# Kernel optimization log

Hardware: AMD Instinct MI355X
Metric: run time of the kernel (lower is better)

Reference implementation:

```python
import jax, jax.numpy as jnp
import numpy as np

G, N, D, H = 2, 192, 64, 4
DK = D // H


def setup_inputs() -> dict:
    key = jax.random.key(0)
    ks = jax.random.split(key, 9)
    s = 0.05
    return {
        "adj": jax.random.normal(ks[0], (G, N, N, D), dtype=jnp.float32),
        "Wq": jax.random.normal(ks[1], (D, D), dtype=jnp.float32) * s,
        "bq": jax.random.normal(ks[2], (D,), dtype=jnp.float32) * s,
        "Wk": jax.random.normal(ks[3], (D, D), dtype=jnp.float32) * s,
        "bk": jax.random.normal(ks[4], (D,), dtype=jnp.float32) * s,
        "Wv": jax.random.normal(ks[5], (D, D), dtype=jnp.float32) * s,
        "bv": jax.random.normal(ks[6], (D,), dtype=jnp.float32) * s,
        "Wo": jax.random.normal(ks[7], (D, D), dtype=jnp.float32) * s,
        "bo": jax.random.normal(ks[8], (D,), dtype=jnp.float32) * s,
    }


def _proj_heads(x, W, b):
    # x: (G,N,N,D) -> (G,N,H,N,DK); W stored as (in,out)
    y = jnp.einsum('gnmd,de->gnme', x, W) + b
    g, n, m, _ = y.shape
    return y.reshape(g, n, m, H, DK).transpose(0, 1, 3, 2, 4)


def reference(adj, Wq, bq, Wk, bk, Wv, bv, Wo, bo):
    q = _proj_heads(adj, Wq, bq)  # (G,N,H,N,DK)
    k = _proj_heads(adj, Wk, bk)
    v = _proj_heads(adj, Wv, bv)
    scores = jnp.einsum('gnhtd,gnhsd->gnhts', q, k) / jnp.sqrt(jnp.float32(DK))
    p = jax.nn.softmax(scores, axis=-1)  # (G,N,H,N,N)
    x = jnp.einsum('gnhts,gnhsd->gnhtd', p, v)  # (G,N,H,N,DK)
    x = x.transpose(0, 1, 3, 2, 4).reshape(adj.shape[0], adj.shape[1], -1, H * DK)
    return jnp.einsum('gnmd,de->gnme', x, Wo) + bo
```

## Files before the change

kernel.cpp:

```cpp
#include <hip/hip_runtime.h>


typedef float    f32x4 __attribute__((ext_vector_type(4)));
typedef float    f32x2 __attribute__((ext_vector_type(2)));
typedef _Float16 f16x2 __attribute__((ext_vector_type(2)));
typedef _Float16 f16x4 __attribute__((ext_vector_type(4)));
typedef _Float16 f16x8 __attribute__((ext_vector_type(8)));

__device__ __forceinline__ int xsw64(int r, int c) {
    return (r << 6) + (((c >> 3) ^ (r & 7)) << 3) + (c & 7);
}
__device__ __forceinline__ int vsw192(int r, int c) {
    return r * 192 + ((((c >> 3) ^ (r & 7)) & 31) << 3) + (c & 7);
}

#define QSCALE 0.36067376022224085f

extern "C" __global__ void spa_prep(const float* __restrict__ Wq, const float* __restrict__ bq,
                                    const float* __restrict__ Wk, const float* __restrict__ bk,
                                    const float* __restrict__ Wv, const float* __restrict__ bv,
                                    const float* __restrict__ Wo, const float* __restrict__ bo,
                                    _Float16* __restrict__ WT, float* __restrict__ BS) {
    const int t = blockIdx.x * 256 + threadIdx.x;
    const int m  = t >> 10;
    const int e  = (t >> 4) & 63;
    const int d0 = (t & 15) << 2;
    const float* W[4] = {Wq, Wk, Wv, Wo};
    const float s = (m == 0) ? QSCALE : 1.0f;
    f16x4 h4;
#pragma unroll
    for (int j = 0; j < 4; ++j) h4[j] = (_Float16)(W[m][(d0 + j) * 64 + e] * s);
    *(f16x4*)&WT[(m << 12) + (e << 6) + d0] = h4;
    if (t < 256) {
        const int mm = t >> 6, ee = t & 63;
        const float* B[4] = {bq, bk, bv, bo};
        BS[t] = B[mm][ee] * ((mm == 0) ? QSCALE : 1.0f);
    }
}

extern "C" __global__ void __launch_bounds__(512, 6)
spa_mfma3(const float* __restrict__ adj,
          const _Float16* __restrict__ WTg, const float* __restrict__ BS,
          float* __restrict__ out) {
    extern __shared__ __align__(16) char smem[];
    _Float16* X  = (_Float16*)smem;
    _Float16* VT = (_Float16*)smem + 12288;

    const int tid  = threadIdx.x;
    const int l    = tid & 63;
    const int wv   = tid >> 6;
    const int l15  = l & 15;
    const int g    = l >> 4;
    const int gn   = blockIdx.x >> 1;
    const int half = blockIdx.x & 1;
    const int ttb  = half * 6;

    const float* Xg   = adj + (size_t)gn * (192 * 64);
    float*       outg = out + (size_t)gn * (192 * 64);

    const int h  = wv >> 1;
    const int eh = h << 4;
    const int et = wv & 3;

    const f16x8 wv0 = *(const f16x8*)&WTg[(2 << 12) + (((et << 4) + l15) << 6) + (g << 3)];
    const f16x8 wv1 = *(const f16x8*)&WTg[(2 << 12) + (((et << 4) + l15) << 6) + 32 + (g << 3)];
    const f16x8 wk0 = *(const f16x8*)&WTg[(1 << 12) + ((eh + l15) << 6) + (g << 3)];
    const f16x8 wk1 = *(const f16x8*)&WTg[(1 << 12) + ((eh + l15) << 6) + 32 + (g << 3)];
    const f16x8 wq0 = *(const f16x8*)&WTg[(0 << 12) + ((eh + l15) << 6) + (g << 3)];
    const f16x8 wq1 = *(const f16x8*)&WTg[(0 << 12) + ((eh + l15) << 6) + 32 + (g << 3)];
    const f32x4 bv4 = *(const f32x4*)&BS[128 + (et << 4) + (g << 2)];
    const f32x4 bk4 = *(const f32x4*)&BS[64 + eh + (g << 2)];
    const f32x4 bq4 = *(const f32x4*)&BS[0 + eh + (g << 2)];

    {
        const int d0 = (tid & 7) << 3;
        const int t0 = tid >> 3;
#pragma unroll
        for (int p = 0; p < 3; ++p) {
            int t = t0 + (p << 6);
            const float4* src = (const float4*)&Xg[(t << 6) + d0];
            float4 v0 = src[0], v1 = src[1];
            f16x8 h8;
            h8[0]=(_Float16)v0.x; h8[1]=(_Float16)v0.y; h8[2]=(_Float16)v0.z; h8[3]=(_Float16)v0.w;
            h8[4]=(_Float16)v1.x; h8[5]=(_Float16)v1.y; h8[6]=(_Float16)v1.z; h8[7]=(_Float16)v1.w;
            *(f16x8*)&X[xsw64(t, d0)] = h8;
        }
    }
    __syncthreads();

    const f32x4 z = {0.f, 0.f, 0.f, 0.f};

    {
        const int stb = (wv >> 2) * 6;
        for (int s6 = 0; s6 < 6; ++s6) {
            int st = stb + s6;
            f16x8 x0 = *(const f16x8*)&X[xsw64((st << 4) + l15, g << 3)];
            f16x8 x1 = *(const f16x8*)&X[xsw64((st << 4) + l15, 32 + (g << 3))];
            f32x4 c = __builtin_amdgcn_mfma_f32_16x16x32_f16(wv0, x0, z, 0, 0, 0);
            c = __builtin_amdgcn_mfma_f32_16x16x32_f16(wv1, x1, c, 0, 0, 0);
            int s = (st << 4) + l15;
#pragma unroll
            for (int r = 0; r < 4; ++r)
                VT[vsw192((et << 4) + (g << 2) + r, s)] = (_Float16)(c[r] + bv4[r]);
        }
    }

    f16x4 kf[12];
#pragma unroll
    for (int st = 0; st < 12; ++st) {
        f16x8 x0 = *(const f16x8*)&X[xsw64((st << 4) + l15, g << 3)];
        f16x8 x1 = *(const f16x8*)&X[xsw64((st << 4) + l15, 32 + (g << 3))];
        f32x4 c = __builtin_amdgcn_mfma_f32_16x16x32_f16(wk0, x0, z, 0, 0, 0);
        c = __builtin_amdgcn_mfma_f32_16x16x32_f16(wk1, x1, c, 0, 0, 0);
#pragma unroll
        for (int r = 0; r < 4; ++r) kf[st][r] = (_Float16)(c[r] + bk4[r]);
    }

    f16x4 qf[3];
    const int tloc = (wv & 1) * 3;
#pragma unroll
    for (int j = 0; j < 3; ++j) {
        int tt = ttb + tloc + j;
        f16x8 x0 = *(const f16x8*)&X[xsw64((tt << 4) + l15, g << 3)];
        f16x8 x1 = *(const f16x8*)&X[xsw64((tt << 4) + l15, 32 + (g << 3))];
        f32x4 c = __builtin_amdgcn_mfma_f32_16x16x32_f16(wq0, x0, z, 0, 0, 0);
        c = __builtin_amdgcn_mfma_f32_16x16x32_f16(wq1, x1, c, 0, 0, 0);
#pragma unroll
        for (int r = 0; r < 4; ++r) qf[j][r] = (_Float16)(c[r] + bq4[r]);
    }
    __syncthreads();

    f16x4 vf[12];
#pragma unroll
    for (int st = 0; st < 12; ++st)
        vf[st] = *(const f16x4*)&VT[vsw192(eh + l15, (st << 4) + (g << 2))];

    for (int j = 0; j < 3; ++j) {
        f32x4 accA = z, accB = z;
        f32x2 rs = {0.f, 0.f};
#pragma unroll
        for (int st = 0; st < 12; ++st) {
            f32x4 c = __builtin_amdgcn_mfma_f32_16x16x16f16(kf[st], qf[j], z, 0, 0, 0);
            float p0 = exp2f(c[0]), p1 = exp2f(c[1]);
            float p2 = exp2f(c[2]), p3 = exp2f(c[3]);
            rs += (f32x2){p0, p1} + (f32x2){p2, p3};
            f16x2 lo = __builtin_bit_cast(f16x2, __builtin_amdgcn_cvt_pkrtz(p0, p1));
            f16x2 hi = __builtin_bit_cast(f16x2, __builtin_amdgcn_cvt_pkrtz(p2, p3));
            f16x4 pf = __builtin_shufflevector(lo, hi, 0, 1, 2, 3);
            if (st & 1) accB = __builtin_amdgcn_mfma_f32_16x16x16f16(vf[st], pf, accB, 0, 0, 0);
            else        accA = __builtin_amdgcn_mfma_f32_16x16x16f16(vf[st], pf, accA, 0, 0, 0);
        }
        float rsum = rs[0] + rs[1];
        rsum += __shfl_xor(rsum, 16);
        rsum += __shfl_xor(rsum, 32);
        const float rinv = 1.0f / rsum;
        f16x4 o4;
#pragma unroll
        for (int r = 0; r < 4; ++r) o4[r] = (_Float16)((accA[r] + accB[r]) * rinv);
        *(f16x4*)&X[xsw64(((ttb + tloc + j) << 4) + l15, eh + (g << 2))] = o4;
    }
    __syncthreads();

    {
        const int eo = ((wv & 3) << 4) + l15;
        const f16x8 wo0 = *(const f16x8*)&WTg[(3 << 12) + (eo << 6) + (g << 3)];
        const f16x8 wo1 = *(const f16x8*)&WTg[(3 << 12) + (eo << 6) + 32 + (g << 3)];
        const float bov = BS[192 + eo];
#pragma unroll
        for (int i = 0; i < 3; ++i) {
            int tt = ttb + ((wv + (i << 3)) >> 2);
            f16x8 a0 = *(const f16x8*)&X[xsw64((tt << 4) + l15, g << 3)];
            f16x8 a1 = *(const f16x8*)&X[xsw64((tt << 4) + l15, 32 + (g << 3))];
            f32x4 c = __builtin_amdgcn_mfma_f32_16x16x32_f16(a0, wo0, z, 0, 0, 0);
            c = __builtin_amdgcn_mfma_f32_16x16x32_f16(a1, wo1, c, 0, 0, 0);
#pragma unroll
            for (int r = 0; r < 4; ++r)
                outg[(((tt << 4) + (g << 2) + r) << 6) + eo] = c[r] + bov;
        }
    }
}

extern "C" void kernel_launch(void* const* d_in, const int* in_sizes, int n_in,
                              void* d_out, int out_size, void* d_ws, size_t ws_size,
                              hipStream_t stream) {
    (void)in_sizes; (void)n_in; (void)ws_size; (void)out_size;
    const float* adj = (const float*)d_in[0];
    _Float16* WT = (_Float16*)d_ws;
    float*    BS = (float*)((char*)d_ws + 32768);

    spa_prep<<<16, 256, 0, stream>>>((const float*)d_in[1], (const float*)d_in[2],
                                     (const float*)d_in[3], (const float*)d_in[4],
                                     (const float*)d_in[5], (const float*)d_in[6],
                                     (const float*)d_in[7], (const float*)d_in[8],
                                     WT, BS);

    const int shmem = 49152;
    spa_mfma3<<<2 * 192 * 2, 512, shmem, stream>>>(adj, WT, BS, (float*)d_out);
}
```

Baseline: 118.9 us.

## Fold weight prep into main kernel and process full query range per block

Removes the separate weight-transpose/convert kernel launch, with each block now loading and converting the fp32 weights to fp16 fragments directly from global memory. The grid is halved so each block handles all 12 query tiles of a (g,n) slice instead of half, so the K and V projections are no longer computed twice per slice. The attention loop is unrolled to process two query tiles per iteration, which interleaves independent MFMA chains. In exchange, register pressure rises (launch bounds drop to 3 waves per EU), weight loads become strided scalar global reads repeated in every block, and fewer blocks are available to fill the device.

```diff
diff --git a/kernel.cpp b/kernel.cpp
--- a/kernel.cpp
+++ b/kernel.cpp
@@ -16,61 +16,48 @@
 
 #define QSCALE 0.36067376022224085f
 
-extern "C" __global__ void spa_prep(const float* __restrict__ Wq, const float* __restrict__ bq,
-                                    const float* __restrict__ Wk, const float* __restrict__ bk,
-                                    const float* __restrict__ Wv, const float* __restrict__ bv,
-                                    const float* __restrict__ Wo, const float* __restrict__ bo,
-                                    _Float16* __restrict__ WT, float* __restrict__ BS) {
-    const int t = blockIdx.x * 256 + threadIdx.x;
-    const int m  = t >> 10;
-    const int e  = (t >> 4) & 63;
-    const int d0 = (t & 15) << 2;
-    const float* W[4] = {Wq, Wk, Wv, Wo};
-    const float s = (m == 0) ? QSCALE : 1.0f;
-    f16x4 h4;
-#pragma unroll
-    for (int j = 0; j < 4; ++j) h4[j] = (_Float16)(W[m][(d0 + j) * 64 + e] * s);
-    *(f16x4*)&WT[(m << 12) + (e << 6) + d0] = h4;
-    if (t < 256) {
-        const int mm = t >> 6, ee = t & 63;
-        const float* B[4] = {bq, bk, bv, bo};
-        BS[t] = B[mm][ee] * ((mm == 0) ? QSCALE : 1.0f);
-    }
-}
-
-extern "C" __global__ void __launch_bounds__(512, 6)
-spa_mfma3(const float* __restrict__ adj,
-          const _Float16* __restrict__ WTg, const float* __restrict__ BS,
+extern "C" __global__ void __launch_bounds__(512, 3)
+spa_mfma4(const float* __restrict__ adj,
+          const float* __restrict__ Wq, const float* __restrict__ bq,
+          const float* __restrict__ Wk, const float* __restrict__ bk,
+          const float* __restrict__ Wv, const float* __restrict__ bv,
+          const float* __restrict__ Wo, const float* __restrict__ bo,
           float* __restrict__ out) {
     extern __shared__ __align__(16) char smem[];
     _Float16* X  = (_Float16*)smem;
     _Float16* VT = (_Float16*)smem + 12288;
 
-    const int tid  = threadIdx.x;
-    const int l    = tid & 63;
-    const int wv   = tid >> 6;
-    const int l15  = l & 15;
-    const int g    = l >> 4;
-    const int gn   = blockIdx.x >> 1;
-    const int half = blockIdx.x & 1;
-    const int ttb  = half * 6;
-
-    const float* Xg   = adj + (size_t)gn * (192 * 64);
-    float*       outg = out + (size_t)gn * (192 * 64);
+    const int tid = threadIdx.x;
+    const int l   = tid & 63;
+    const int wv  = tid >> 6;
+    const int l15 = l & 15;
+    const int g   = l >> 4;
+
+    const float* Xg   = adj + (size_t)blockIdx.x * (192 * 64);
+    float*       outg = out + (size_t)blockIdx.x * (192 * 64);
 
     const int h  = wv >> 1;
     const int eh = h << 4;
     const int et = wv & 3;
-
-    const f16x8 wv0 = *(const f16x8*)&WTg[(2 << 12) + (((et << 4) + l15) << 6) + (g << 3)];
-    const f16x8 wv1 = *(const f16x8*)&WTg[(2 << 12) + (((et << 4) + l15) << 6) + 32 + (g << 3)];
-    const f16x8 wk0 = *(const f16x8*)&WTg[(1 << 12) + ((eh + l15) << 6) + (g << 3)];
-    const f16x8 wk1 = *(const f16x8*)&WTg[(1 << 12) + ((eh + l15) << 6) + 32 + (g << 3)];
-    const f16x8 wq0 = *(const f16x8*)&WTg[(0 << 12) + ((eh + l15) << 6) + (g << 3)];
-    const f16x8 wq1 = *(const f16x8*)&WTg[(0 << 12) + ((eh + l15) << 6) + 32 + (g << 3)];
-    const f32x4 bv4 = *(const f32x4*)&BS[128 + (et << 4) + (g << 2)];
-    const f32x4 bk4 = *(const f32x4*)&BS[64 + eh + (g << 2)];
-    const f32x4 bq4 = *(const f32x4*)&BS[0 + eh + (g << 2)];
+    const int ew = eh + l15;
+    const int ev = ((wv & 3) << 4) + l15;
+
+    f16x8 wq0, wq1, wk0, wk1, wvv0, wvv1;
+#pragma unroll
+    for (int jd = 0; jd < 8; ++jd) {
+        const int d0 = (g << 3) + jd;
+        wq0[jd]  = (_Float16)(Wq[d0 * 64 + ew] * QSCALE);
+        wq1[jd]  = (_Float16)(Wq[(32 + d0) * 64 + ew] * QSCALE);
+        wk0[jd]  = (_Float16)(Wk[d0 * 64 + ew]);
+        wk1[jd]  = (_Float16)(Wk[(32 + d0) * 64 + ew]);
+        wvv0[jd] = (_Float16)(Wv[d0 * 64 + ev]);
+        wvv1[jd] = (_Float16)(Wv[(32 + d0) * 64 + ev]);
+    }
+    f32x4 bq4 = *(const f32x4*)&bq[eh + (g << 2)];
+#pragma unroll
+    for (int r = 0; r < 4; ++r) bq4[r] *= QSCALE;
+    const f32x4 bk4 = *(const f32x4*)&bk[eh + (g << 2)];
+    const f32x4 bv4 = *(const f32x4*)&bv[((wv & 3) << 4) + (g << 2)];
 
     {
         const int d0 = (tid & 7) << 3;
@@ -96,8 +83,8 @@
             int st = stb + s6;
             f16x8 x0 = *(const f16x8*)&X[xsw64((st << 4) + l15, g << 3)];
             f16x8 x1 = *(const f16x8*)&X[xsw64((st << 4) + l15, 32 + (g << 3))];
-            f32x4 c = __builtin_amdgcn_mfma_f32_16x16x32_f16(wv0, x0, z, 0, 0, 0);
-            c = __builtin_amdgcn_mfma_f32_16x16x32_f16(wv1, x1, c, 0, 0, 0);
+            f32x4 c = __builtin_amdgcn_mfma_f32_16x16x32_f16(wvv0, x0, z, 0, 0, 0);
+            c = __builtin_amdgcn_mfma_f32_16x16x32_f16(wvv1, x1, c, 0, 0, 0);
             int s = (st << 4) + l15;
 #pragma unroll
             for (int r = 0; r < 4; ++r)
@@ -116,11 +103,11 @@
         for (int r = 0; r < 4; ++r) kf[st][r] = (_Float16)(c[r] + bk4[r]);
     }
 
-    f16x4 qf[3];
-    const int tloc = (wv & 1) * 3;
-#pragma unroll
-    for (int j = 0; j < 3; ++j) {
-        int tt = ttb + tloc + j;
+    f16x4 qf[6];
+    const int tloc = (wv & 1) * 6;
+#pragma unroll
+    for (int j = 0; j < 6; ++j) {
+        int tt = tloc + j;
         f16x8 x0 = *(const f16x8*)&X[xsw64((tt << 4) + l15, g << 3)];
         f16x8 x1 = *(const f16x8*)&X[xsw64((tt << 4) + l15, 32 + (g << 3))];
         f32x4 c = __builtin_amdgcn_mfma_f32_16x16x32_f16(wq0, x0, z, 0, 0, 0);
@@ -130,45 +117,71 @@
     }
     __syncthreads();
 
+    f16x8 wo0, wo1;
+#pragma unroll
+    for (int jd = 0; jd < 8; ++jd) {
+        const int d0 = (g << 3) + jd;
+        wo0[jd] = (_Float16)(Wo[d0 * 64 + ev]);
+        wo1[jd] = (_Float16)(Wo[(32 + d0) * 64 + ev]);
+    }
+    const float bov = bo[ev];
+
     f16x4 vf[12];
 #pragma unroll
     for (int st = 0; st < 12; ++st)
         vf[st] = *(const f16x4*)&VT[vsw192(eh + l15, (st << 4) + (g << 2))];
 
-    for (int j = 0; j < 3; ++j) {
-        f32x4 accA = z, accB = z;
-        f32x2 rs = {0.f, 0.f};
+#pragma unroll
+    for (int jj = 0; jj < 3; ++jj) {
+        const int j0 = 2 * jj, j1 = 2 * jj + 1;
+        f32x4 accA0 = z, accB0 = z, accA1 = z, accB1 = z;
+        f32x2 rs0 = {0.f, 0.f}, rs1 = {0.f, 0.f};
 #pragma unroll
         for (int st = 0; st < 12; ++st) {
-            f32x4 c = __builtin_amdgcn_mfma_f32_16x16x16f16(kf[st], qf[j], z, 0, 0, 0);
-            float p0 = exp2f(c[0]), p1 = exp2f(c[1]);
-            float p2 = exp2f(c[2]), p3 = exp2f(c[3]);
-            rs += (f32x2){p0, p1} + (f32x2){p2, p3};
-            f16x2 lo = __builtin_bit_cast(f16x2, __builtin_amdgcn_cvt_pkrtz(p0, p1));
-            f16x2 hi = __builtin_bit_cast(f16x2, __builtin_amdgcn_cvt_pkrtz(p2, p3));
-            f16x4 pf = __builtin_shufflevector(lo, hi, 0, 1, 2, 3);
-            if (st & 1) accB = __builtin_amdgcn_mfma_f32_16x16x16f16(vf[st], pf, accB, 0, 0, 0);
-            else        accA = __builtin_amdgcn_mfma_f32_16x16x16f16(vf[st], pf, accA, 0, 0, 0);
-        }
-        float rsum = rs[0] + rs[1];
-        rsum += __shfl_xor(rsum, 16);
-        rsum += __shfl_xor(rsum, 32);
-        const float rinv = 1.0f / rsum;
-        f16x4 o4;
-#pragma unroll
-        for (int r = 0; r < 4; ++r) o4[r] = (_Float16)((accA[r] + accB[r]) * rinv);
-        *(f16x4*)&X[xsw64(((ttb + tloc + j) << 4) + l15, eh + (g << 2))] = o4;
+            f32x4 c0 = __builtin_amdgcn_mfma_f32_16x16x16f16(kf[st], qf[j0], z, 0, 0, 0);
+            f32x4 c1 = __builtin_amdgcn_mfma_f32_16x16x16f16(kf[st], qf[j1], z, 0, 0, 0);
+            float p00 = exp2f(c0[0]), p01 = exp2f(c0[1]), p02 = exp2f(c0[2]), p03 = exp2f(c0[3]);
+            float p10 = exp2f(c1[0]), p11 = exp2f(c1[1]), p12 = exp2f(c1[2]), p13 = exp2f(c1[3]);
+            rs0 += (f32x2){p00, p01} + (f32x2){p02, p03};
+            rs1 += (f32x2){p10, p11} + (f32x2){p12, p13};
+            f16x2 lo0 = __builtin_bit_cast(f16x2, __builtin_amdgcn_cvt_pkrtz(p00, p01));
+            f16x2 hi0 = __builtin_bit_cast(f16x2, __builtin_amdgcn_cvt_pkrtz(p02, p03));
+            f16x2 lo1 = __builtin_bit_cast(f16x2, __builtin_amdgcn_cvt_pkrtz(p10, p11));
+            f16x2 hi1 = __builtin_bit_cast(f16x2, __builtin_amdgcn_cvt_pkrtz(p12, p13));
+            f16x4 pf0 = __builtin_shufflevector(lo0, hi0, 0, 1, 2, 3);
+            f16x4 pf1 = __builtin_shufflevector(lo1, hi1, 0, 1, 2, 3);
+            if (st & 1) {
+                accB0 = __builtin_amdgcn_mfma_f32_16x16x16f16(vf[st], pf0, accB0, 0, 0, 0);
+                accB1 = __builtin_amdgcn_mfma_f32_16x16x16f16(vf[st], pf1, accB1, 0, 0, 0);
+            } else {
+                accA0 = __builtin_amdgcn_mfma_f32_16x16x16f16(vf[st], pf0, accA0, 0, 0, 0);
+                accA1 = __builtin_amdgcn_mfma_f32_16x16x16f16(vf[st], pf1, accA1, 0, 0, 0);
+            }
+        }
+        float rsum0 = rs0[0] + rs0[1];
+        float rsum1 = rs1[0] + rs1[1];
+        rsum0 += __shfl_xor(rsum0, 16);
+        rsum0 += __shfl_xor(rsum0, 32);
+        rsum1 += __shfl_xor(rsum1, 16);
+        rsum1 += __shfl_xor(rsum1, 32);
+        const float rinv0 = 1.0f / rsum0;
+        const float rinv1 = 1.0f / rsum1;
+        f16x4 o0, o1;
+#pragma unroll
+        for (int r = 0; r < 4; ++r) {
+            o0[r] = (_Float16)((accA0[r] + accB0[r]) * rinv0);
+            o1[r] = (_Float16)((accA1[r] + accB1[r]) * rinv1);
+        }
+        *(f16x4*)&X[xsw64(((tloc + j0) << 4) + l15, eh + (g << 2))] = o0;
+        *(f16x4*)&X[xsw64(((tloc + j1) << 4) + l15, eh + (g << 2))] = o1;
     }
     __syncthreads();
 
     {
-        const int eo = ((wv & 3) << 4) + l15;
-        const f16x8 wo0 = *(const f16x8*)&WTg[(3 << 12) + (eo << 6) + (g << 3)];
-        const f16x8 wo1 = *(const f16x8*)&WTg[(3 << 12) + (eo << 6) + 32 + (g << 3)];
-        const float bov = BS[192 + eo];
-#pragma unroll
-        for (int i = 0; i < 3; ++i) {
-            int tt = ttb + ((wv + (i << 3)) >> 2);
+        const int eo = ev;
+#pragma unroll
+        for (int i = 0; i < 6; ++i) {
+            int tt = (wv + (i << 3)) >> 2;
             f16x8 a0 = *(const f16x8*)&X[xsw64((tt << 4) + l15, g << 3)];
             f16x8 a1 = *(const f16x8*)&X[xsw64((tt << 4) + l15, 32 + (g << 3))];
             f32x4 c = __builtin_amdgcn_mfma_f32_16x16x32_f16(a0, wo0, z, 0, 0, 0);
@@ -183,17 +196,13 @@
 extern "C" void kernel_launch(void* const* d_in, const int* in_sizes, int n_in,
                               void* d_out, int out_size, void* d_ws, size_t ws_size,
                               hipStream_t stream) {
-    (void)in_sizes; (void)n_in; (void)ws_size; (void)out_size;
-    const float* adj = (const float*)d_in[0];
-    _Float16* WT = (_Float16*)d_ws;
-    float*    BS = (float*)((char*)d_ws + 32768);
-
-    spa_prep<<<16, 256, 0, stream>>>((const float*)d_in[1], (const float*)d_in[2],
-                                     (const float*)d_in[3], (const float*)d_in[4],
-                                     (const float*)d_in[5], (const float*)d_in[6],
-                                     (const float*)d_in[7], (const float*)d_in[8],
-                                     WT, BS);
-
+    (void)in_sizes; (void)n_in; (void)d_ws; (void)ws_size; (void)out_size;
     const int shmem = 49152;
-    spa_mfma3<<<2 * 192 * 2, 512, shmem, stream>>>(adj, WT, BS, (float*)d_out);
-}
+    spa_mfma4<<<2 * 192, 512, shmem, stream>>>(
+        (const float*)d_in[0],
+        (const float*)d_in[1], (const float*)d_in[2],
+        (const float*)d_in[3], (const float*)d_in[4],
+        (const float*)d_in[5], (const float*)d_in[6],
+        (const float*)d_in[7], (const float*)d_in[8],
+        (float*)d_out);
+}
```

Result: faster. 113.6 us (-4.5%).
